# Kernel tuning notes

Measured on AMD Instinct MI355X. Metric: run time of the kernel, lower is better.

## Reference

```python
import jax, jax.numpy as jnp
import numpy as np

N = 1024        # nodes per tree (= sentence length)
VOCAB = 100000
IN_DIM = 300
MEM = 300
HID = 200
CLS = 5


def _make_parents(rng):
    # post-order tree: every node's parent has a larger index; node N-1 is root
    p = np.empty(N, dtype=np.int64)
    for n in range(N - 1):
        p[n] = rng.integers(n + 1, N)
    p[N - 1] = N - 1  # root points to itself; its scatter is never read
    return jnp.asarray(p)


def _linear_params(key, fin, fout):
    kw, kb = jax.random.split(key)
    lim = 1.0 / np.sqrt(fin)
    W = jax.random.uniform(kw, (fout, fin), minval=-lim, maxval=lim, dtype=jnp.float32)
    b = jax.random.uniform(kb, (fout,), minval=-lim, maxval=lim, dtype=jnp.float32)
    return W, b


def setup_inputs() -> dict:
    key = jax.random.key(0)
    ks = jax.random.split(key, 9)
    rng = np.random.default_rng(0)
    lparents = _make_parents(rng)
    rparents = _make_parents(rng)
    lsent = jax.random.randint(ks[0], (N,), 0, VOCAB)
    rsent = jax.random.randint(ks[1], (N,), 0, VOCAB)
    emb = jax.random.normal(ks[2], (VOCAB, IN_DIM), dtype=jnp.float32) * 0.02
    emb = emb.at[0].set(0.0)  # padding_idx = 0
    Wioux, bioux = _linear_params(ks[3], IN_DIM, 3 * MEM)
    Wiouh, biouh = _linear_params(ks[4], MEM, 3 * MEM)
    Wfx, bfx = _linear_params(ks[5], IN_DIM, MEM)
    Wfh, bfh = _linear_params(ks[6], MEM, MEM)
    Wwh, bwh = _linear_params(ks[7], 2 * MEM, HID)
    Wwp, bwp = _linear_params(ks[8], HID, CLS)
    return {
        'lsent': lsent, 'lparents': lparents,
        'rsent': rsent, 'rparents': rparents,
        'calculate_sim': 0,
        'emb': emb,
        'Wioux': Wioux, 'bioux': bioux, 'Wiouh': Wiouh, 'biouh': biouh,
        'Wfx': Wfx, 'bfx': bfx, 'Wfh': Wfh, 'bfh': bfh,
        'Wwh': Wwh, 'bwh': bwh, 'Wwp': Wwp, 'bwp': bwp,
    }


def _tree_lstm(x, parents, Wioux, bioux, Wiouh, biouh, Wfx, bfx, Wfh, bfh):
    # x: [N, in_dim]; parents: [N] with parent idx > node idx (post-order)
    n_nodes = x.shape[0]
    mem = Wfh.shape[0]
    xiou = x @ Wioux.T + bioux  # [N, 3M] input part of i,o,u gates (precomputed)
    xf = x @ Wfx.T + bfx        # [N, M]  input part of forget gate (per PARENT)

    def step(carry, n):
        hsum, fcsum = carry  # [N,M] accumulated sum of children h / f*c per node
        iou = xiou[n] + hsum[n] @ Wiouh.T + biouh
        i, o, u = jnp.split(iou, 3)
        i, o, u = jax.nn.sigmoid(i), jax.nn.sigmoid(o), jnp.tanh(u)
        c = i * u + fcsum[n]
        h = o * jnp.tanh(c)
        p = parents[n]
        # child-sum scatter to parent: f = sigmoid(fh(h_child) + fx(x_parent))
        f = jax.nn.sigmoid(h @ Wfh.T + bfh + xf[p])
        carry = (hsum.at[p].add(h), fcsum.at[p].add(f * c))
        return carry, h

    init = (jnp.zeros((n_nodes, mem), x.dtype), jnp.zeros((n_nodes, mem), x.dtype))
    _, hs = jax.lax.scan(step, init, jnp.arange(n_nodes))
    return hs  # [N, M]; root hidden is hs[-1]


def reference(lsent, lparents, rsent, rparents, calculate_sim, emb,
              Wioux, bioux, Wiouh, biouh, Wfx, bfx, Wfh, bfh,
              Wwh, bwh, Wwp, bwp):
    lx = emb[lsent]  # [N, in_dim]
    rx = emb[rsent]
    lh = _tree_lstm(lx, lparents, Wioux, bioux, Wiouh, biouh, Wfx, bfx, Wfh, bfh)
    rh = _tree_lstm(rx, rparents, Wioux, bioux, Wiouh, biouh, Wfx, bfx, Wfh, bfh)
    lvec = lh[-1:]  # [1, M] root hidden state
    rvec = rh[-1:]
    vec_dist = jnp.concatenate([lvec * rvec, jnp.abs(lvec - rvec)], axis=1)
    hid = jax.nn.sigmoid(vec_dist @ Wwh.T + bwh)
    out = jax.nn.log_softmax(hid @ Wwp.T + bwp, axis=1)  # [1, num_classes]
    return out, lh, rh
```

## Files before the change

kernel.cpp:

```cpp
#include <hip/hip_runtime.h>
#include <math.h>

#define NN 1024
#define MEM 300
#define SLICE 20
#define GB 15
#define NG 8
#define BPT (GB * NG)
#define SCAN_T 512

__device__ __forceinline__ float agloadf(const float* p) {
  return __hip_atomic_load(p, __ATOMIC_RELAXED, __HIP_MEMORY_SCOPE_AGENT);
}
__device__ __forceinline__ void agstoref(float* p, float v) {
  __hip_atomic_store(p, v, __ATOMIC_RELAXED, __HIP_MEMORY_SCOPE_AGENT);
}

__device__ __forceinline__ void treebar(int* bar, int t) {
  __syncthreads();
  if (threadIdx.x == 0) {
    int* cnt = bar + t * 32;
    int* gen = bar + t * 32 + 16;
    __threadfence();
    int g = __hip_atomic_load(gen, __ATOMIC_RELAXED, __HIP_MEMORY_SCOPE_AGENT);
    int v = __hip_atomic_fetch_add(cnt, 1, __ATOMIC_ACQ_REL, __HIP_MEMORY_SCOPE_AGENT);
    if (v == BPT - 1) {
      __hip_atomic_store(cnt, 0, __ATOMIC_RELAXED, __HIP_MEMORY_SCOPE_AGENT);
      __hip_atomic_fetch_add(gen, 1, __ATOMIC_RELEASE, __HIP_MEMORY_SCOPE_AGENT);
    } else {
      while (__hip_atomic_load(gen, __ATOMIC_ACQUIRE, __HIP_MEMORY_SCOPE_AGENT) == g) {
        __builtin_amdgcn_s_sleep(2);
      }
    }
    __threadfence();
  }
  __syncthreads();
}

__device__ __forceinline__ float sigmoidf_(float x) {
  return 1.0f / (1.0f + expf(-x));
}

__global__ __launch_bounds__(1024, 1)
void levels_kernel(const int* __restrict__ lparents, const int* __restrict__ rparents,
                   int* __restrict__ list, int* __restrict__ offsG, int* __restrict__ mlG,
                   int* __restrict__ childOff, int* __restrict__ childList) {
  const int t = blockIdx.x;
  const int* par = t ? rparents : lparents;
  const int n = threadIdx.x;
  __shared__ int lvlS[NN];
  __shared__ int aux[NN];
  __shared__ int coff[NN];
  __shared__ int cnts[64];
  __shared__ int offsS[65];
  __shared__ int curL[64];
  __shared__ int chunk[32];
  __shared__ int flagS;
  const int p = par[n];
  lvlS[n] = 0; aux[n] = 0;
  if (n < 64) { cnts[n] = 0; curL[n] = 0; }
  __syncthreads();
  for (int it = 0; it < 64; ++it) {
    if (n == 0) flagS = 0;
    __syncthreads();
    if (n < NN - 1) {
      int v = lvlS[n] + 1;
      int old = atomicMax(&lvlS[p], v);
      if (old < v) flagS = 1;
    }
    __syncthreads();
    if (!flagS) break;
  }
  const int L = lvlS[n];
  atomicAdd(&cnts[L], 1);
  if (n < NN - 1) atomicAdd(&aux[p], 1);
  __syncthreads();
  if (n == 0) {
    int acc = 0;
    for (int l = 0; l < 64; ++l) { offsS[l] = acc; acc += cnts[l]; }
    offsS[64] = acc;
    mlG[t] = lvlS[NN - 1];
  }
  __syncthreads();
  { int pos = atomicAdd(&curL[L], 1); list[t * NN + offsS[L] + pos] = n; }
  if (n < 32) { int s = 0; for (int i = 0; i < 32; ++i) s += aux[n * 32 + i]; chunk[n] = s; }
  __syncthreads();
  if (n == 0) { int acc = 0; for (int i = 0; i < 32; ++i) { int s = chunk[i]; chunk[i] = acc; acc += s; } }
  __syncthreads();
  if (n < 32) { int acc = chunk[n]; for (int i = 0; i < 32; ++i) { coff[n * 32 + i] = acc; acc += aux[n * 32 + i]; } }
  __syncthreads();
  childOff[t * (NN + 1) + n] = coff[n];
  if (n == 0) childOff[t * (NN + 1) + NN] = NN - 1;
  aux[n] = 0;
  __syncthreads();
  if (n < NN - 1) { int idx = coff[p] + atomicAdd(&aux[p], 1); childList[t * NN + idx] = n; }
  if (n < 65) offsG[t * 65 + n] = offsS[n];
}

#define K1_NT 32
#define K1_CT 48
__global__ __launch_bounds__(256, 1)
void proj_kernel(const int* __restrict__ lsent, const int* __restrict__ rsent,
                 const float* __restrict__ emb,
                 const float* __restrict__ Wioux, const float* __restrict__ bioux,
                 const float* __restrict__ Wfx, const float* __restrict__ bfx,
                 float* __restrict__ xiou, float* __restrict__ xf) {
  __shared__ float xt[K1_NT][300];
  __shared__ float wt[K1_CT][100];
  const int tid = threadIdx.x;
  const int g0 = blockIdx.y * K1_NT;
  const int c0 = blockIdx.x * K1_CT;

  for (int e = tid; e < K1_NT * 300; e += 256) {
    int nn = e / 300, k = e - nn * 300;
    int g = g0 + nn;
    int t = g >> 10, n = g & (NN - 1);
    int s = (t ? rsent : lsent)[n];
    xt[nn][k] = emb[(size_t)s * 300 + k];
  }

  const int a = tid >> 4;
  const int b = tid & 15;
  float acc00 = 0, acc01 = 0, acc02 = 0, acc10 = 0, acc11 = 0, acc12 = 0;

  for (int kc = 0; kc < 300; kc += 100) {
    __syncthreads();
    for (int e = tid; e < K1_CT * 100; e += 256) {
      int cc = e / 100, k = e - cc * 100;
      int col = c0 + cc;
      wt[cc][k] = (col < 900) ? Wioux[(size_t)col * 300 + kc + k]
                              : Wfx[(size_t)(col - 900) * 300 + kc + k];
    }
    __syncthreads();
    #pragma unroll
    for (int k4 = 0; k4 < 25; ++k4) {
      float4 x0 = *(const float4*)&xt[a][kc + k4 * 4];
      float4 x1 = *(const float4*)&xt[a + 16][kc + k4 * 4];
      float4 w0 = *(const float4*)&wt[b][k4 * 4];
      float4 w1 = *(const float4*)&wt[b + 16][k4 * 4];
      float4 w2 = *(const float4*)&wt[b + 32][k4 * 4];
      acc00 += x0.x * w0.x + x0.y * w0.y + x0.z * w0.z + x0.w * w0.w;
      acc01 += x0.x * w1.x + x0.y * w1.y + x0.z * w1.z + x0.w * w1.w;
      acc02 += x0.x * w2.x + x0.y * w2.y + x0.z * w2.z + x0.w * w2.w;
      acc10 += x1.x * w0.x + x1.y * w0.y + x1.z * w0.z + x1.w * w0.w;
      acc11 += x1.x * w1.x + x1.y * w1.y + x1.z * w1.z + x1.w * w1.w;
      acc12 += x1.x * w2.x + x1.y * w2.y + x1.z * w2.z + x1.w * w2.w;
    }
  }

  float accs[2][3] = {{acc00, acc01, acc02}, {acc10, acc11, acc12}};
  for (int ni = 0; ni < 2; ++ni) {
    for (int ci = 0; ci < 3; ++ci) {
      int g = g0 + a + 16 * ni;
      int col = c0 + b + 16 * ci;
      int t = g >> 10, n = g & (NN - 1);
      float v = accs[ni][ci];
      if (col < 900) xiou[((size_t)t * NN + n) * 900 + col] = v + bioux[col];
      else           xf[((size_t)t * NN + n) * 300 + (col - 900)] = v + bfx[col - 900];
    }
  }
}

__global__ __launch_bounds__(SCAN_T, 1)
void scan_kernel(const float* __restrict__ Wiouh, const float* __restrict__ biouh,
                 const float* __restrict__ Wfh, const float* __restrict__ bfh,
                 const float* __restrict__ xiou, const float* __restrict__ xf,
                 const int* __restrict__ list, const int* __restrict__ offsG,
                 const int* __restrict__ mlG, const int* __restrict__ childOff,
                 const int* __restrict__ childList,
                 float* cbuf, int* bar, float* out) {
  const int tid = threadIdx.x;
  const int t = blockIdx.x / BPT;
  const int b = blockIdx.x % BPT;
  const int colb = b % GB;
  const int gg = b / GB;
  const int j0 = colb * SLICE;

  const int slot = tid >> 4;
  const int ks = tid & 15;
  const int kk0 = ks * 19;
  const bool dotT = (tid < 320);

  const float* xiouT = xiou + (size_t)t * NN * 900;
  const float* xfT = xf + (size_t)t * NN * MEM;
  float* cbufT = cbuf + (size_t)t * NN * MEM;
  float* hT = out + 5 + (size_t)t * NN * MEM;
  const int* listT = list + t * NN;
  const int* coT = childOff + t * (NN + 1);
  const int* clT = childList + t * NN;

  float w0[19], w1[19], w2[19], w3[19];
  if (dotT) {
    const float* r0 = Wiouh + (size_t)(j0 + slot) * MEM;
    const float* r1 = Wiouh + (size_t)(MEM + j0 + slot) * MEM;
    const float* r2 = Wiouh + (size_t)(2 * MEM + j0 + slot) * MEM;
    const float* r3 = Wfh + (size_t)(j0 + slot) * MEM;
    #pragma unroll
    for (int i = 0; i < 19; ++i) {
      const int k = kk0 + i;
      const bool ok = (k < 300);
      const int kc = ok ? k : 0;
      w0[i] = ok ? r0[kc] : 0.f;
      w1[i] = ok ? r1[kc] : 0.f;
      w2[i] = ok ? r2[kc] : 0.f;
      w3[i] = ok ? r3[kc] : 0.f;
    }
  } else {
    #pragma unroll
    for (int i = 0; i < 19; ++i) { w0[i] = w1[i] = w2[i] = w3[i] = 0.f; }
  }

  __shared__ float vb[4][304];
  __shared__ float hsumS[4][304];
  __shared__ float fcS[4][SLICE];
  __shared__ float xiS[4][3][SLICE];
  __shared__ float xfS[4][SLICE];
  __shared__ float cslc[4][SLICE];
  __shared__ float dfS[4][SLICE];
  __shared__ float dIS[4][SLICE], dOS[4][SLICE], dUS[4][SLICE];
  __shared__ int nodeId[4], cS_[4], cE_[4], fOff[5], bbc[4], chc[4];
  __shared__ int offsS[65];
  __shared__ float bI[SLICE], bO[SLICE], bU[SLICE], bF[SLICE];

  if (tid < SLICE) {
    bI[tid] = biouh[j0 + tid];
    bO[tid] = biouh[300 + j0 + tid];
    bU[tid] = biouh[600 + j0 + tid];
    bF[tid] = bfh[j0 + tid];
  }
  if (tid < 65) offsS[tid] = offsG[t * 65 + tid];
  __syncthreads();
  const int ml = mlG[t];

  {
    const int c0l = offsS[0], cn = offsS[1] - offsS[0];
    for (int base = gg * 24; base < cn; base += 24 * NG) {
      const int nb = min(24, cn - base);
      if (tid < nb * SLICE) {
        int bb = tid / SLICE, j = tid - bb * SLICE;
        int n = listT[c0l + base + bb];
        const float* xr = xiouT + (size_t)n * 900;
        float i_ = sigmoidf_(xr[j0 + j] + bI[j]);
        float o_ = sigmoidf_(xr[300 + j0 + j] + bO[j]);
        float u_ = tanhf(xr[600 + j0 + j] + bU[j]);
        float c = i_ * u_;
        float h = o_ * tanhf(c);
        agstoref(&cbufT[(size_t)n * MEM + j0 + j], c);
        agstoref(&hT[(size_t)n * MEM + j0 + j], h);
      }
    }
    treebar(bar, t);
  }

  for (int L = 1; L <= ml; ++L) {
    const int c0l = offsS[L], cn = offsS[L + 1] - offsS[L];
    for (int base = gg * 4; base < cn; base += 4 * NG) {
      const int nb = min(4, cn - base);
      for (int e = tid; e < 4 * 304; e += SCAN_T) ((float*)hsumS)[e] = 0.f;
      if (tid < 4 * SLICE) ((float*)fcS)[tid] = 0.f;
      if (tid < nb) {
        int n = listT[c0l + base + tid];
        nodeId[tid] = n;
        cS_[tid] = coT[n];
        cE_[tid] = coT[n + 1];
      }
      __syncthreads();
      if (tid == 0) {
        int acc = 0;
        for (int bb = 0; bb < nb; ++bb) { fOff[bb] = acc; acc += cE_[bb] - cS_[bb]; }
        fOff[nb] = acc;
      }
      for (int e = tid; e < nb * 3 * SLICE; e += SCAN_T) {
        int bb = e / (3 * SLICE), r = e % (3 * SLICE), g = r / SLICE, j = r % SLICE;
        xiS[bb][g][j] = xiouT[(size_t)nodeId[bb] * 900 + g * 300 + j0 + j];
      }
      if (tid < nb * SLICE) {
        int bb = tid / SLICE, j = tid % SLICE;
        xfS[bb][j] = xfT[(size_t)nodeId[bb] * MEM + j0 + j];
      }
      __syncthreads();
      const int tc = fOff[nb];
      for (int cs = 0; cs < tc; cs += 4) {
        const int nc = min(4, tc - cs);
        if (tid < nc) {
          int idx = cs + tid, bb = 0;
          while (idx >= fOff[bb + 1]) ++bb;
          bbc[tid] = bb;
          chc[tid] = clT[cS_[bb] + idx - fOff[bb]];
        }
        __syncthreads();
        for (int e = tid; e < nc * 304; e += SCAN_T) {
          int cc = e / 304, k = e - cc * 304;
          vb[cc][k] = (k < 300) ? agloadf(&hT[(size_t)chc[cc] * MEM + k]) : 0.f;
        }
        if (tid < nc * SLICE) {
          int cc = tid / SLICE, j = tid % SLICE;
          cslc[cc][j] = agloadf(&cbufT[(size_t)chc[cc] * MEM + j0 + j]);
        }
        __syncthreads();
        if (dotT) {
          for (int cc = 0; cc < nc; ++cc) {
            float a = 0.f;
            #pragma unroll
            for (int i = 0; i < 19; ++i) a += w3[i] * vb[cc][kk0 + i];
            a += __shfl_xor(a, 1); a += __shfl_xor(a, 2);
            a += __shfl_xor(a, 4); a += __shfl_xor(a, 8);
            if (ks == 0) dfS[cc][slot] = a;
          }
        } else {
          for (int k = tid - 320; k < 304; k += 192)
            for (int cc = 0; cc < nc; ++cc) hsumS[bbc[cc]][k] += vb[cc][k];
        }
        __syncthreads();
        if (tid < nc * SLICE) {
          int cc = tid / SLICE, j = tid % SLICE, bb = bbc[cc];
          float f = sigmoidf_(dfS[cc][j] + bF[j] + xfS[bb][j]);
          atomicAdd(&fcS[bb][j], f * cslc[cc][j]);
        }
        __syncthreads();
      }
      if (dotT) {
        for (int bb = 0; bb < nb; ++bb) {
          float aI = 0.f, aO = 0.f, aU = 0.f;
          #pragma unroll
          for (int i = 0; i < 19; ++i) {
            float v = hsumS[bb][kk0 + i];
            aI += w0[i] * v; aO += w1[i] * v; aU += w2[i] * v;
          }
          aI += __shfl_xor(aI, 1); aO += __shfl_xor(aO, 1); aU += __shfl_xor(aU, 1);
          aI += __shfl_xor(aI, 2); aO += __shfl_xor(aO, 2); aU += __shfl_xor(aU, 2);
          aI += __shfl_xor(aI, 4); aO += __shfl_xor(aO, 4); aU += __shfl_xor(aU, 4);
          aI += __shfl_xor(aI, 8); aO += __shfl_xor(aO, 8); aU += __shfl_xor(aU, 8);
          if (ks == 0) { dIS[bb][slot] = aI; dOS[bb][slot] = aO; dUS[bb][slot] = aU; }
        }
      }
      __syncthreads();
      if (tid < nb * SLICE) {
        int bb = tid / SLICE, j = tid % SLICE;
        int n = nodeId[bb];
        float i_ = sigmoidf_(dIS[bb][j] + bI[j] + xiS[bb][0][j]);
        float o_ = sigmoidf_(dOS[bb][j] + bO[j] + xiS[bb][1][j]);
        float u_ = tanhf(dUS[bb][j] + bU[j] + xiS[bb][2][j]);
        float c = i_ * u_ + fcS[bb][j];
        float h = o_ * tanhf(c);
        agstoref(&cbufT[(size_t)n * MEM + j0 + j], c);
        agstoref(&hT[(size_t)n * MEM + j0 + j], h);
      }
      __syncthreads();
    }
    treebar(bar, t);
  }
}

__global__ __launch_bounds__(256, 1)
void head_kernel(const float* __restrict__ Wwh, const float* __restrict__ bwh,
                 const float* __restrict__ Wwp, const float* __restrict__ bwp,
                 float* out) {
  __shared__ float vd[600];
  __shared__ float hid[200];
  __shared__ float sL[5];
  const int tid = threadIdx.x;
  for (int e = tid; e < 300; e += 256) {
    float lv = out[5 + 1023 * 300 + e];
    float rv = out[5 + 307200 + 1023 * 300 + e];
    vd[e] = lv * rv;
    vd[300 + e] = fabsf(lv - rv);
  }
  __syncthreads();
  if (tid < 200) {
    float acc = bwh[tid];
    const float* wr = Wwh + (size_t)tid * 600;
    for (int k = 0; k < 600; ++k) acc += vd[k] * wr[k];
    hid[tid] = sigmoidf_(acc);
  }
  __syncthreads();
  if (tid < 5) {
    float acc = bwp[tid];
    const float* wr = Wwp + (size_t)tid * 200;
    for (int k = 0; k < 200; ++k) acc += hid[k] * wr[k];
    sL[tid] = acc;
  }
  __syncthreads();
  if (tid == 0) {
    float m = sL[0];
    for (int c = 1; c < 5; ++c) m = fmaxf(m, sL[c]);
    float s = 0.f;
    for (int c = 0; c < 5; ++c) s += expf(sL[c] - m);
    float lz = m + logf(s);
    for (int c = 0; c < 5; ++c) out[c] = sL[c] - lz;
  }
}

extern "C" void kernel_launch(void* const* d_in, const int* in_sizes, int n_in,
                              void* d_out, int out_size, void* d_ws, size_t ws_size,
                              hipStream_t stream) {
  const int* lsent = (const int*)d_in[0];
  const int* lparents = (const int*)d_in[1];
  const int* rsent = (const int*)d_in[2];
  const int* rparents = (const int*)d_in[3];
  const float* emb = (const float*)d_in[5];
  const float* Wioux = (const float*)d_in[6];
  const float* bioux = (const float*)d_in[7];
  const float* Wiouh = (const float*)d_in[8];
  const float* biouh = (const float*)d_in[9];
  const float* Wfx = (const float*)d_in[10];
  const float* bfx = (const float*)d_in[11];
  const float* Wfh = (const float*)d_in[12];
  const float* bfh = (const float*)d_in[13];
  const float* Wwh = (const float*)d_in[14];
  const float* bwh = (const float*)d_in[15];
  const float* Wwp = (const float*)d_in[16];
  const float* bwp = (const float*)d_in[17];
  float* out = (float*)d_out;

  char* ws = (char*)d_ws;
  int* bar = (int*)(ws);
  float* cbuf = (float*)(ws + 256);
  int* list = (int*)(ws + 2457856);
  int* offsG = (int*)(ws + 2466048);
  int* mlG = (int*)(ws + 2466816);
  int* childOff = (int*)(ws + 2467072);
  int* childList = (int*)(ws + 2475520);
  float* xiou = (float*)(ws + 2483712);
  float* xf = (float*)(ws + 9856512);

  hipMemsetAsync(ws, 0, 256, stream);
  levels_kernel<<<2, 1024, 0, stream>>>(lparents, rparents, list, offsG, mlG,
                                        childOff, childList);
  proj_kernel<<<dim3(25, 64), 256, 0, stream>>>(lsent, rsent, emb, Wioux, bioux,
                                                Wfx, bfx, xiou, xf);
  scan_kernel<<<2 * BPT, SCAN_T, 0, stream>>>(Wiouh, biouh, Wfh, bfh, xiou, xf,
                                              list, offsG, mlG, childOff, childList,
                                              cbuf, bar, out);
  head_kernel<<<1, 256, 0, stream>>>(Wwh, bwh, Wwp, bwp, out);
}
```

Baseline: 1.037 ms.

## Replace level-synchronous grid barriers with per-node dataflow readiness counters

Drops the level computation and the grid-wide barrier between tree levels. Each node is now processed by a fixed block group (nodes assigned round-robin) that spins on per-child ready counters, so independent subtrees can proceed without waiting for a whole level. The column slice and group sizes change (more groups, wider slices), and launch bounds now allow several blocks per CU. This gives up batching of several nodes per step and relies on spin-waiting, which needs all 384 blocks co-resident to avoid deadlock.

```diff
diff --git a/kernel.cpp b/kernel.cpp
--- a/kernel.cpp
+++ b/kernel.cpp
@@ -3,9 +3,9 @@
 
 #define NN 1024
 #define MEM 300
-#define SLICE 20
-#define GB 15
-#define NG 8
+#define SLICE 25
+#define GB 12
+#define NG 16
 #define BPT (GB * NG)
 #define SCAN_T 512
 
@@ -16,73 +16,24 @@
   __hip_atomic_store(p, v, __ATOMIC_RELAXED, __HIP_MEMORY_SCOPE_AGENT);
 }
 
-__device__ __forceinline__ void treebar(int* bar, int t) {
-  __syncthreads();
-  if (threadIdx.x == 0) {
-    int* cnt = bar + t * 32;
-    int* gen = bar + t * 32 + 16;
-    __threadfence();
-    int g = __hip_atomic_load(gen, __ATOMIC_RELAXED, __HIP_MEMORY_SCOPE_AGENT);
-    int v = __hip_atomic_fetch_add(cnt, 1, __ATOMIC_ACQ_REL, __HIP_MEMORY_SCOPE_AGENT);
-    if (v == BPT - 1) {
-      __hip_atomic_store(cnt, 0, __ATOMIC_RELAXED, __HIP_MEMORY_SCOPE_AGENT);
-      __hip_atomic_fetch_add(gen, 1, __ATOMIC_RELEASE, __HIP_MEMORY_SCOPE_AGENT);
-    } else {
-      while (__hip_atomic_load(gen, __ATOMIC_ACQUIRE, __HIP_MEMORY_SCOPE_AGENT) == g) {
-        __builtin_amdgcn_s_sleep(2);
-      }
-    }
-    __threadfence();
-  }
-  __syncthreads();
-}
-
 __device__ __forceinline__ float sigmoidf_(float x) {
   return 1.0f / (1.0f + expf(-x));
 }
 
 __global__ __launch_bounds__(1024, 1)
-void levels_kernel(const int* __restrict__ lparents, const int* __restrict__ rparents,
-                   int* __restrict__ list, int* __restrict__ offsG, int* __restrict__ mlG,
-                   int* __restrict__ childOff, int* __restrict__ childList) {
+void csr_kernel(const int* __restrict__ lparents, const int* __restrict__ rparents,
+                int* __restrict__ childOff, int* __restrict__ childList) {
   const int t = blockIdx.x;
   const int* par = t ? rparents : lparents;
   const int n = threadIdx.x;
-  __shared__ int lvlS[NN];
   __shared__ int aux[NN];
   __shared__ int coff[NN];
-  __shared__ int cnts[64];
-  __shared__ int offsS[65];
-  __shared__ int curL[64];
   __shared__ int chunk[32];
-  __shared__ int flagS;
   const int p = par[n];
-  lvlS[n] = 0; aux[n] = 0;
-  if (n < 64) { cnts[n] = 0; curL[n] = 0; }
-  __syncthreads();
-  for (int it = 0; it < 64; ++it) {
-    if (n == 0) flagS = 0;
-    __syncthreads();
-    if (n < NN - 1) {
-      int v = lvlS[n] + 1;
-      int old = atomicMax(&lvlS[p], v);
-      if (old < v) flagS = 1;
-    }
-    __syncthreads();
-    if (!flagS) break;
-  }
-  const int L = lvlS[n];
-  atomicAdd(&cnts[L], 1);
+  aux[n] = 0;
+  __syncthreads();
   if (n < NN - 1) atomicAdd(&aux[p], 1);
   __syncthreads();
-  if (n == 0) {
-    int acc = 0;
-    for (int l = 0; l < 64; ++l) { offsS[l] = acc; acc += cnts[l]; }
-    offsS[64] = acc;
-    mlG[t] = lvlS[NN - 1];
-  }
-  __syncthreads();
-  { int pos = atomicAdd(&curL[L], 1); list[t * NN + offsS[L] + pos] = n; }
   if (n < 32) { int s = 0; for (int i = 0; i < 32; ++i) s += aux[n * 32 + i]; chunk[n] = s; }
   __syncthreads();
   if (n == 0) { int acc = 0; for (int i = 0; i < 32; ++i) { int s = chunk[i]; chunk[i] = acc; acc += s; } }
@@ -94,7 +45,6 @@
   aux[n] = 0;
   __syncthreads();
   if (n < NN - 1) { int idx = coff[p] + atomicAdd(&aux[p], 1); childList[t * NN + idx] = n; }
-  if (n < 65) offsG[t * 65 + n] = offsS[n];
 }
 
 #define K1_NT 32
@@ -161,14 +111,12 @@
   }
 }
 
-__global__ __launch_bounds__(SCAN_T, 1)
+__global__ __launch_bounds__(SCAN_T, 4)
 void scan_kernel(const float* __restrict__ Wiouh, const float* __restrict__ biouh,
                  const float* __restrict__ Wfh, const float* __restrict__ bfh,
                  const float* __restrict__ xiou, const float* __restrict__ xf,
-                 const int* __restrict__ list, const int* __restrict__ offsG,
-                 const int* __restrict__ mlG, const int* __restrict__ childOff,
-                 const int* __restrict__ childList,
-                 float* cbuf, int* bar, float* out) {
+                 const int* __restrict__ childOff, const int* __restrict__ childList,
+                 int* rdy, float* cbuf, float* out) {
   const int tid = threadIdx.x;
   const int t = blockIdx.x / BPT;
   const int b = blockIdx.x % BPT;
@@ -179,15 +127,15 @@
   const int slot = tid >> 4;
   const int ks = tid & 15;
   const int kk0 = ks * 19;
-  const bool dotT = (tid < 320);
+  const bool dotT = (slot < SLICE);
 
   const float* xiouT = xiou + (size_t)t * NN * 900;
   const float* xfT = xf + (size_t)t * NN * MEM;
   float* cbufT = cbuf + (size_t)t * NN * MEM;
   float* hT = out + 5 + (size_t)t * NN * MEM;
-  const int* listT = list + t * NN;
   const int* coT = childOff + t * (NN + 1);
   const int* clT = childList + t * NN;
+  int* rdyT = rdy + t * NN;
 
   float w0[19], w1[19], w2[19], w3[19];
   if (dotT) {
@@ -211,15 +159,13 @@
   }
 
   __shared__ float vb[4][304];
-  __shared__ float hsumS[4][304];
-  __shared__ float fcS[4][SLICE];
-  __shared__ float xiS[4][3][SLICE];
-  __shared__ float xfS[4][SLICE];
+  __shared__ float hsumS[304];
+  __shared__ float fcS[SLICE];
+  __shared__ float xfS[SLICE];
   __shared__ float cslc[4][SLICE];
   __shared__ float dfS[4][SLICE];
-  __shared__ float dIS[4][SLICE], dOS[4][SLICE], dUS[4][SLICE];
-  __shared__ int nodeId[4], cS_[4], cE_[4], fOff[5], bbc[4], chc[4];
-  __shared__ int offsS[65];
+  __shared__ float dIS[SLICE], dOS[SLICE], dUS[SLICE];
+  __shared__ int chc[4];
   __shared__ float bI[SLICE], bO[SLICE], bU[SLICE], bF[SLICE];
 
   if (tid < SLICE) {
@@ -228,127 +174,102 @@
     bU[tid] = biouh[600 + j0 + tid];
     bF[tid] = bfh[j0 + tid];
   }
-  if (tid < 65) offsS[tid] = offsG[t * 65 + tid];
-  __syncthreads();
-  const int ml = mlG[t];
-
-  {
-    const int c0l = offsS[0], cn = offsS[1] - offsS[0];
-    for (int base = gg * 24; base < cn; base += 24 * NG) {
-      const int nb = min(24, cn - base);
-      if (tid < nb * SLICE) {
-        int bb = tid / SLICE, j = tid - bb * SLICE;
-        int n = listT[c0l + base + bb];
+  __syncthreads();
+
+  for (int n = gg; n < NN; n += NG) {
+    const int cS = coT[n];
+    const int nchild = coT[n + 1] - cS;
+
+    if (nchild == 0) {
+      if (tid < SLICE) {
         const float* xr = xiouT + (size_t)n * 900;
-        float i_ = sigmoidf_(xr[j0 + j] + bI[j]);
-        float o_ = sigmoidf_(xr[300 + j0 + j] + bO[j]);
-        float u_ = tanhf(xr[600 + j0 + j] + bU[j]);
+        float i_ = sigmoidf_(xr[j0 + tid] + bI[tid]);
+        float o_ = sigmoidf_(xr[300 + j0 + tid] + bO[tid]);
+        float u_ = tanhf(xr[600 + j0 + tid] + bU[tid]);
         float c = i_ * u_;
         float h = o_ * tanhf(c);
-        agstoref(&cbufT[(size_t)n * MEM + j0 + j], c);
-        agstoref(&hT[(size_t)n * MEM + j0 + j], h);
-      }
-    }
-    treebar(bar, t);
-  }
-
-  for (int L = 1; L <= ml; ++L) {
-    const int c0l = offsS[L], cn = offsS[L + 1] - offsS[L];
-    for (int base = gg * 4; base < cn; base += 4 * NG) {
-      const int nb = min(4, cn - base);
-      for (int e = tid; e < 4 * 304; e += SCAN_T) ((float*)hsumS)[e] = 0.f;
-      if (tid < 4 * SLICE) ((float*)fcS)[tid] = 0.f;
-      if (tid < nb) {
-        int n = listT[c0l + base + tid];
-        nodeId[tid] = n;
-        cS_[tid] = coT[n];
-        cE_[tid] = coT[n + 1];
-      }
-      __syncthreads();
-      if (tid == 0) {
-        int acc = 0;
-        for (int bb = 0; bb < nb; ++bb) { fOff[bb] = acc; acc += cE_[bb] - cS_[bb]; }
-        fOff[nb] = acc;
-      }
-      for (int e = tid; e < nb * 3 * SLICE; e += SCAN_T) {
-        int bb = e / (3 * SLICE), r = e % (3 * SLICE), g = r / SLICE, j = r % SLICE;
-        xiS[bb][g][j] = xiouT[(size_t)nodeId[bb] * 900 + g * 300 + j0 + j];
-      }
-      if (tid < nb * SLICE) {
-        int bb = tid / SLICE, j = tid % SLICE;
-        xfS[bb][j] = xfT[(size_t)nodeId[bb] * MEM + j0 + j];
-      }
-      __syncthreads();
-      const int tc = fOff[nb];
-      for (int cs = 0; cs < tc; cs += 4) {
-        const int nc = min(4, tc - cs);
-        if (tid < nc) {
-          int idx = cs + tid, bb = 0;
-          while (idx >= fOff[bb + 1]) ++bb;
-          bbc[tid] = bb;
-          chc[tid] = clT[cS_[bb] + idx - fOff[bb]];
+        agstoref(&cbufT[(size_t)n * MEM + j0 + tid], c);
+        agstoref(&hT[(size_t)n * MEM + j0 + tid], h);
+      }
+      __syncthreads();
+      if (tid == 0)
+        __hip_atomic_fetch_add(&rdyT[n], 1, __ATOMIC_RELEASE, __HIP_MEMORY_SCOPE_AGENT);
+      continue;
+    }
+
+    for (int e = tid; e < 304; e += SCAN_T) hsumS[e] = 0.f;
+    if (tid >= 304 && tid < 304 + SLICE) fcS[tid - 304] = 0.f;
+    if (tid >= 352 && tid < 352 + SLICE)
+      xfS[tid - 352] = xfT[(size_t)n * MEM + j0 + (tid - 352)];
+    for (int i = tid; i < nchild; i += SCAN_T) {
+      const int ch = clT[cS + i];
+      while (__hip_atomic_load(&rdyT[ch], __ATOMIC_ACQUIRE, __HIP_MEMORY_SCOPE_AGENT) < GB)
+        __builtin_amdgcn_s_sleep(1);
+    }
+    __syncthreads();
+
+    for (int cs = 0; cs < nchild; cs += 4) {
+      const int nc = min(4, nchild - cs);
+      if (tid < nc) chc[tid] = clT[cS + cs + tid];
+      __syncthreads();
+      for (int e = tid; e < nc * 304; e += SCAN_T) {
+        int cc = e / 304, k = e - cc * 304;
+        vb[cc][k] = (k < 300) ? agloadf(&hT[(size_t)chc[cc] * MEM + k]) : 0.f;
+      }
+      if (tid < nc * SLICE) {
+        int cc = tid / SLICE, j = tid % SLICE;
+        cslc[cc][j] = agloadf(&cbufT[(size_t)chc[cc] * MEM + j0 + j]);
+      }
+      __syncthreads();
+      if (dotT) {
+        for (int cc = 0; cc < nc; ++cc) {
+          float a = 0.f;
+          #pragma unroll
+          for (int i = 0; i < 19; ++i) a += w3[i] * vb[cc][kk0 + i];
+          a += __shfl_xor(a, 1); a += __shfl_xor(a, 2);
+          a += __shfl_xor(a, 4); a += __shfl_xor(a, 8);
+          if (ks == 0) dfS[cc][slot] = a;
         }
-        __syncthreads();
-        for (int e = tid; e < nc * 304; e += SCAN_T) {
-          int cc = e / 304, k = e - cc * 304;
-          vb[cc][k] = (k < 300) ? agloadf(&hT[(size_t)chc[cc] * MEM + k]) : 0.f;
-        }
-        if (tid < nc * SLICE) {
-          int cc = tid / SLICE, j = tid % SLICE;
-          cslc[cc][j] = agloadf(&cbufT[(size_t)chc[cc] * MEM + j0 + j]);
-        }
-        __syncthreads();
-        if (dotT) {
-          for (int cc = 0; cc < nc; ++cc) {
-            float a = 0.f;
-            #pragma unroll
-            for (int i = 0; i < 19; ++i) a += w3[i] * vb[cc][kk0 + i];
-            a += __shfl_xor(a, 1); a += __shfl_xor(a, 2);
-            a += __shfl_xor(a, 4); a += __shfl_xor(a, 8);
-            if (ks == 0) dfS[cc][slot] = a;
-          }
-        } else {
-          for (int k = tid - 320; k < 304; k += 192)
-            for (int cc = 0; cc < nc; ++cc) hsumS[bbc[cc]][k] += vb[cc][k];
-        }
-        __syncthreads();
-        if (tid < nc * SLICE) {
-          int cc = tid / SLICE, j = tid % SLICE, bb = bbc[cc];
-          float f = sigmoidf_(dfS[cc][j] + bF[j] + xfS[bb][j]);
-          atomicAdd(&fcS[bb][j], f * cslc[cc][j]);
-        }
-        __syncthreads();
-      }
-      if (dotT) {
-        for (int bb = 0; bb < nb; ++bb) {
-          float aI = 0.f, aO = 0.f, aU = 0.f;
-          #pragma unroll
-          for (int i = 0; i < 19; ++i) {
-            float v = hsumS[bb][kk0 + i];
-            aI += w0[i] * v; aO += w1[i] * v; aU += w2[i] * v;
-          }
-          aI += __shfl_xor(aI, 1); aO += __shfl_xor(aO, 1); aU += __shfl_xor(aU, 1);
-          aI += __shfl_xor(aI, 2); aO += __shfl_xor(aO, 2); aU += __shfl_xor(aU, 2);
-          aI += __shfl_xor(aI, 4); aO += __shfl_xor(aO, 4); aU += __shfl_xor(aU, 4);
-          aI += __shfl_xor(aI, 8); aO += __shfl_xor(aO, 8); aU += __shfl_xor(aU, 8);
-          if (ks == 0) { dIS[bb][slot] = aI; dOS[bb][slot] = aO; dUS[bb][slot] = aU; }
-        }
-      }
-      __syncthreads();
-      if (tid < nb * SLICE) {
-        int bb = tid / SLICE, j = tid % SLICE;
-        int n = nodeId[bb];
-        float i_ = sigmoidf_(dIS[bb][j] + bI[j] + xiS[bb][0][j]);
-        float o_ = sigmoidf_(dOS[bb][j] + bO[j] + xiS[bb][1][j]);
-        float u_ = tanhf(dUS[bb][j] + bU[j] + xiS[bb][2][j]);
-        float c = i_ * u_ + fcS[bb][j];
-        float h = o_ * tanhf(c);
-        agstoref(&cbufT[(size_t)n * MEM + j0 + j], c);
-        agstoref(&hT[(size_t)n * MEM + j0 + j], h);
-      }
-      __syncthreads();
-    }
-    treebar(bar, t);
+      } else {
+        for (int k = tid - 400; k < 304; k += 112)
+          for (int cc = 0; cc < nc; ++cc) hsumS[k] += vb[cc][k];
+      }
+      __syncthreads();
+      if (tid < nc * SLICE) {
+        int cc = tid / SLICE, j = tid % SLICE;
+        float f = sigmoidf_(dfS[cc][j] + bF[j] + xfS[j]);
+        atomicAdd(&fcS[j], f * cslc[cc][j]);
+      }
+      __syncthreads();
+    }
+
+    if (dotT) {
+      float aI = 0.f, aO = 0.f, aU = 0.f;
+      #pragma unroll
+      for (int i = 0; i < 19; ++i) {
+        float v = hsumS[kk0 + i];
+        aI += w0[i] * v; aO += w1[i] * v; aU += w2[i] * v;
+      }
+      aI += __shfl_xor(aI, 1); aO += __shfl_xor(aO, 1); aU += __shfl_xor(aU, 1);
+      aI += __shfl_xor(aI, 2); aO += __shfl_xor(aO, 2); aU += __shfl_xor(aU, 2);
+      aI += __shfl_xor(aI, 4); aO += __shfl_xor(aO, 4); aU += __shfl_xor(aU, 4);
+      aI += __shfl_xor(aI, 8); aO += __shfl_xor(aO, 8); aU += __shfl_xor(aU, 8);
+      if (ks == 0) { dIS[slot] = aI; dOS[slot] = aO; dUS[slot] = aU; }
+    }
+    __syncthreads();
+    if (tid < SLICE) {
+      const float* xr = xiouT + (size_t)n * 900;
+      float i_ = sigmoidf_(dIS[tid] + bI[tid] + xr[j0 + tid]);
+      float o_ = sigmoidf_(dOS[tid] + bO[tid] + xr[300 + j0 + tid]);
+      float u_ = tanhf(dUS[tid] + bU[tid] + xr[600 + j0 + tid]);
+      float c = i_ * u_ + fcS[tid];
+      float h = o_ * tanhf(c);
+      agstoref(&cbufT[(size_t)n * MEM + j0 + tid], c);
+      agstoref(&hT[(size_t)n * MEM + j0 + tid], h);
+    }
+    __syncthreads();
+    if (tid == 0)
+      __hip_atomic_fetch_add(&rdyT[n], 1, __ATOMIC_RELEASE, __HIP_MEMORY_SCOPE_AGENT);
   }
 }
 
@@ -414,23 +335,18 @@
   float* out = (float*)d_out;
 
   char* ws = (char*)d_ws;
-  int* bar = (int*)(ws);
-  float* cbuf = (float*)(ws + 256);
-  int* list = (int*)(ws + 2457856);
-  int* offsG = (int*)(ws + 2466048);
-  int* mlG = (int*)(ws + 2466816);
-  int* childOff = (int*)(ws + 2467072);
-  int* childList = (int*)(ws + 2475520);
-  float* xiou = (float*)(ws + 2483712);
-  float* xf = (float*)(ws + 9856512);
-
-  hipMemsetAsync(ws, 0, 256, stream);
-  levels_kernel<<<2, 1024, 0, stream>>>(lparents, rparents, list, offsG, mlG,
-                                        childOff, childList);
+  int* rdy = (int*)(ws);
+  float* cbuf = (float*)(ws + 8192);
+  int* childOff = (int*)(ws + 2465792);
+  int* childList = (int*)(ws + 2474112);
+  float* xiou = (float*)(ws + 2482304);
+  float* xf = (float*)(ws + 9855104);
+
+  hipMemsetAsync(ws, 0, 8192, stream);
+  csr_kernel<<<2, 1024, 0, stream>>>(lparents, rparents, childOff, childList);
   proj_kernel<<<dim3(25, 64), 256, 0, stream>>>(lsent, rsent, emb, Wioux, bioux,
                                                 Wfx, bfx, xiou, xf);
   scan_kernel<<<2 * BPT, SCAN_T, 0, stream>>>(Wiouh, biouh, Wfh, bfh, xiou, xf,
-                                              list, offsG, mlG, childOff, childList,
-                                              cbuf, bar, out);
+                                              childOff, childList, rdy, cbuf, out);
   head_kernel<<<1, 256, 0, stream>>>(Wwh, bwh, Wwp, bwp, out);
 }
```

New measurement: 1.134 ms. 1.09x slower.
